# Optimization experiments

Measured on AMD Instinct MI355X. Metric: run time of the kernel, lower is better.

## Reference

```python
import jax, jax.numpy as jnp
import numpy as np

B, S, E, H = 2, 1024, 4096, 16
D = E // H          # head_dim = 256
RD = 64             # rotary_dim
# Quantization scales (alpha of the int8 GEMM epilogues)
A_QKV = 1.2e-4      # W8A8B8O8 q/k/v projection output scale
A_QK = 2e-4         # BMM_S8T_S8N_F32T alpha (= q_scale * k_scale)
A_PV = 1.0 / 127.0  # BMM_S8T_S8N_S8T alpha (probs quantized by *127)
A_O = 0.01          # W8A8BFP32OFP32 out_proj alpha


def setup_inputs() -> dict:
    key = jax.random.key(0)
    ks = jax.random.split(key, 9)
    ri = lambda k, shp: jax.random.randint(k, shp, -127, 128).astype(jnp.float32)
    return {
        "hidden_states": ri(ks[0], (B, S, E)),   # int8-valued activations
        "Wq": ri(ks[1], (E, E)),
        "Wk": ri(ks[2], (E, E)),
        "Wv": ri(ks[3], (E, E)),
        "Wo": ri(ks[4], (E, E)),
        "bq": ri(ks[5], (E,)),
        "bk": ri(ks[6], (E,)),
        "bv": ri(ks[7], (E,)),
        "bo": jax.random.normal(ks[8], (E,), dtype=jnp.float32) * 0.02,  # fp32 bias
    }


def _linear_i8(x, W, b, alpha):
    # W8A8B8O8Linear: int8 GEMM, scaled, +int8 bias, round+saturate to int8
    y = alpha * (x @ W.T) + b
    return jnp.clip(jnp.round(y), -128, 127)


def _rotate_every_two(x):
    x1 = x[..., ::2]
    x2 = x[..., 1::2]
    return jnp.stack((-x2, x1), axis=-1).reshape(x.shape)


def _apply_rotary(x, sin, cos):
    # duplicate_interleave == repeat each column twice; broadcast over [B, S, H, rd]
    sin = jnp.repeat(sin, 2, axis=-1)[None, :, None, :]
    cos = jnp.repeat(cos, 2, axis=-1)[None, :, None, :]
    r = x * cos + _rotate_every_two(x) * sin
    # torch: clamp(-128,127).to(int8) -> truncate toward zero
    return jnp.trunc(jnp.clip(r, -128.0, 127.0))


def reference(hidden_states, Wq, Wk, Wv, Wo, bq, bk, bv, bo):
    q = _linear_i8(hidden_states, Wq, bq, A_QKV).reshape(B, S, H, D)
    k = _linear_i8(hidden_states, Wk, bk, A_QKV).reshape(B, S, H, D)
    v = _linear_i8(hidden_states, Wv, bv, A_QKV).reshape(B, S, H, D)
    v = v.transpose(0, 2, 1, 3)  # [B, H, S, D]

    # fixed_pos_embedding over rotary_dim
    inv_freq = 1.0 / (10000.0 ** (jnp.arange(0, RD, 2, dtype=jnp.float32) / RD))
    t = jnp.arange(S, dtype=jnp.float32)
    sinusoid = t[:, None] * inv_freq[None, :]   # [S, RD/2]
    sin, cos = jnp.sin(sinusoid), jnp.cos(sinusoid)

    q = jnp.concatenate([_apply_rotary(q[..., :RD], sin, cos), q[..., RD:]], axis=-1)
    k = jnp.concatenate([_apply_rotary(k[..., :RD], sin, cos), k[..., RD:]], axis=-1)
    q = q.transpose(0, 2, 1, 3)  # [B, H, S, D]
    k = k.transpose(0, 2, 1, 3)

    w = A_QK * jnp.einsum('bhqd,bhkd->bhqk', q, k)
    causal = jnp.tril(jnp.ones((S, S), dtype=bool))[None, None]
    w = jnp.where(causal, w, jnp.finfo(jnp.float32).min)
    w = w / jnp.sqrt(jnp.float32(D))  # scale_attn = sqrt(head_dim)
    p = jnp.round(jax.nn.softmax(w, axis=-1) * 127.0)  # int8-valued probs

    # pv_bmm: int8 probs x int8 values -> scaled, round+saturate to int8
    o = jnp.clip(jnp.round(A_PV * jnp.einsum('bhqk,bhkd->bhqd', p, v)), -128, 127)
    o = o.transpose(0, 2, 1, 3).reshape(B, S, E)  # merge heads

    # out_proj: W8A8BFP32OFP32 -> fp32 output
    return A_O * (o @ Wo.T) + bo
```

## Files before the change

### kernel.cpp

```cpp
#include <hip/hip_runtime.h>
#include <hip/hip_bf16.h>

typedef int int32x4 __attribute__((ext_vector_type(4)));
typedef signed char i8;

#define B_ 2
#define S_ 1024
#define E_ 4096
#define H_ 16
#define D_ 256

#define MFMA_I8(a, b, c) __builtin_amdgcn_mfma_i32_16x16x64_i8((a), (b), (c), 0, 0, 0)

__device__ __forceinline__ int32x4 ld16(const void* p) {
    return *reinterpret_cast<const int32x4*>(p);
}

__device__ __forceinline__ void gload16(const void* g, void* l) {
    __builtin_amdgcn_global_load_lds(
        (const __attribute__((address_space(1))) void*)g,
        (__attribute__((address_space(3))) void*)l, 16, 0, 0);
}

#define WAIT_VM4()  asm volatile("s_waitcnt vmcnt(4)" ::: "memory")
#define WAIT_VM0()  asm volatile("s_waitcnt vmcnt(0)" ::: "memory")
#define WAIT_LGKM0() do { asm volatile("s_waitcnt lgkmcnt(0)" ::: "memory"); \
                          __builtin_amdgcn_sched_barrier(0); } while (0)

__device__ __forceinline__ int pack4(float4 f) {
    union { int w; i8 b[4]; } u;
    u.b[0] = (i8)f.x; u.b[1] = (i8)f.y; u.b[2] = (i8)f.z; u.b[3] = (i8)f.w;
    return u.w;
}

__global__ void k_f32_to_i8(const float* __restrict__ src, i8* __restrict__ dst, int n4) {
    int i = blockIdx.x * blockDim.x + threadIdx.x;
    if (i >= n4) return;
    reinterpret_cast<int*>(dst)[i] = pack4(reinterpret_cast<const float4*>(src)[i]);
}

__global__ void k_w_to_i8(const float* __restrict__ w0, const float* __restrict__ w1,
                          const float* __restrict__ w2, const float* __restrict__ w3,
                          i8* __restrict__ d0, i8* __restrict__ d1,
                          i8* __restrict__ d2, i8* __restrict__ d3, int n4) {
    int i = blockIdx.x * blockDim.x + threadIdx.x;
    if (i >= n4) return;
    const float* src = (blockIdx.y == 0) ? w0 : (blockIdx.y == 1) ? w1 : (blockIdx.y == 2) ? w2 : w3;
    i8* dst = (blockIdx.y == 0) ? d0 : (blockIdx.y == 1) ? d1 : (blockIdx.y == 2) ? d2 : d3;
    reinterpret_cast<int*>(dst)[i] = pack4(reinterpret_cast<const float4*>(src)[i]);
}

__global__ void k_sincos(float* __restrict__ sin_t, float* __restrict__ cos_t) {
    int idx = blockIdx.x * blockDim.x + threadIdx.x;
    if (idx >= S_ * 32) return;
    int s = idx >> 5, i = idx & 31;
    float ex = (float)(2 * i) / 64.0f;
    float invf = 1.0f / powf(10000.0f, ex);
    float arg = (float)s * invf;
    sin_t[idx] = (float)sin((double)arg);
    cos_t[idx] = (float)cos((double)arg);
}

template<bool OUT_I8>
__device__ __forceinline__ void gemm_core(
    const i8* __restrict__ X, const i8* __restrict__ W, const float* __restrict__ bias,
    void* __restrict__ out, float alpha, int M, int N, int K,
    i8 (&Alds)[3][8192], i8 (&Blds)[3][8192])
{
    const int nt = K >> 6;
    const int nwg = (M >> 7) * (N >> 7);
    const int q = nwg >> 3;
    const int lin = blockIdx.x;
    const int wg = (lin & 7) * q + (lin >> 3);
    const int nbm = M >> 7;
    const int m0 = (wg % nbm) * 128, n0 = (wg / nbm) * 128;

    const int tid = threadIdx.x, lane = tid & 63, wave = tid >> 6;
    const int wr = wave >> 1, wc = wave & 1, l4 = lane & 15, lh = lane >> 4;

    const int g4 = lh ^ ((l4 >> 1) & 3);
    const int aoff = (wr * 64 + l4) * 64 + g4 * 16;
    const int boff = (wc * 64 + l4) * 64 + g4 * 16;

    const int srow = tid >> 2;
    const int sg = (tid & 3) ^ ((tid >> 3) & 3);
    const i8* Asrc = X + (size_t)(m0 + srow) * K + sg * 16;
    const i8* Bsrc = W + (size_t)(n0 + srow) * K + sg * 16;
    const size_t rstep = (size_t)64 * K;
    const int ldst = wave * 1024;

#define STAGE_A(t_) do { int kb_ = (t_) * 64; i8* lb_ = Alds[(t_) % 3];      \
        gload16(Asrc + kb_,         lb_ + ldst);                             \
        gload16(Asrc + rstep + kb_, lb_ + 4096 + ldst); } while (0)
#define STAGE_B(t_) do { int kb_ = (t_) * 64; i8* lb_ = Blds[(t_) % 3];      \
        gload16(Bsrc + kb_,         lb_ + ldst);                             \
        gload16(Bsrc + rstep + kb_, lb_ + 4096 + ldst); } while (0)

    int32x4 acc[4][4];
#pragma unroll
    for (int m = 0; m < 4; ++m)
#pragma unroll
        for (int n = 0; n < 4; ++n) acc[m][n] = int32x4{0, 0, 0, 0};

    STAGE_A(0); STAGE_B(0);
    STAGE_A(1); STAGE_B(1);

    for (int t = 0; t < nt; ++t) {
        const i8* Ab = Alds[t % 3];
        const i8* Bb = Blds[t % 3];
        if (t + 1 < nt) { WAIT_VM4(); } else { WAIT_VM0(); }
        __builtin_amdgcn_s_barrier();

        int32x4 a0, a1, a2, a3, b0, b1, b2, b3;
        a0 = ld16(Ab + aoff);        a1 = ld16(Ab + aoff + 1024);
        a2 = ld16(Ab + aoff + 2048); a3 = ld16(Ab + aoff + 3072);
        b0 = ld16(Bb + boff);        b1 = ld16(Bb + boff + 1024);
        if (t + 2 < nt) STAGE_A(t + 2);
        __builtin_amdgcn_s_barrier();
        WAIT_LGKM0();
        __builtin_amdgcn_s_setprio(1);
        acc[0][0] = MFMA_I8(a0, b0, acc[0][0]);
        acc[1][0] = MFMA_I8(a1, b0, acc[1][0]);
        acc[2][0] = MFMA_I8(a2, b0, acc[2][0]);
        acc[3][0] = MFMA_I8(a3, b0, acc[3][0]);
        acc[0][1] = MFMA_I8(a0, b1, acc[0][1]);
        acc[1][1] = MFMA_I8(a1, b1, acc[1][1]);
        acc[2][1] = MFMA_I8(a2, b1, acc[2][1]);
        acc[3][1] = MFMA_I8(a3, b1, acc[3][1]);
        __builtin_amdgcn_s_setprio(0);
        __builtin_amdgcn_s_barrier();

        b2 = ld16(Bb + boff + 2048); b3 = ld16(Bb + boff + 3072);
        if (t + 2 < nt) STAGE_B(t + 2);
        __builtin_amdgcn_s_barrier();
        WAIT_LGKM0();
        __builtin_amdgcn_s_setprio(1);
        acc[0][2] = MFMA_I8(a0, b2, acc[0][2]);
        acc[1][2] = MFMA_I8(a1, b2, acc[1][2]);
        acc[2][2] = MFMA_I8(a2, b2, acc[2][2]);
        acc[3][2] = MFMA_I8(a3, b2, acc[3][2]);
        acc[0][3] = MFMA_I8(a0, b3, acc[0][3]);
        acc[1][3] = MFMA_I8(a1, b3, acc[1][3]);
        acc[2][3] = MFMA_I8(a2, b3, acc[2][3]);
        acc[3][3] = MFMA_I8(a3, b3, acc[3][3]);
        __builtin_amdgcn_s_setprio(0);
    }
#undef STAGE_A
#undef STAGE_B

#pragma unroll
    for (int m = 0; m < 4; ++m)
#pragma unroll
        for (int n = 0; n < 4; ++n)
#pragma unroll
            for (int r = 0; r < 4; ++r) {
                int grow = m0 + wr * 64 + m * 16 + lh * 4 + r;
                int gcol = n0 + wc * 64 + n * 16 + l4;
                float y = alpha * (float)acc[m][n][r] + bias[gcol];
                if (OUT_I8) {
                    float v = rintf(y);
                    v = fminf(fmaxf(v, -128.0f), 127.0f);
                    reinterpret_cast<i8*>(out)[(size_t)grow * N + gcol] = (i8)v;
                } else {
                    reinterpret_cast<float*>(out)[(size_t)grow * N + gcol] = y;
                }
            }
}

__global__ __launch_bounds__(256) void k_gemm_qkv(
    const i8* __restrict__ X,
    const i8* __restrict__ w0, const i8* __restrict__ w1, const i8* __restrict__ w2,
    const float* __restrict__ b0, const float* __restrict__ b1, const float* __restrict__ b2,
    i8* __restrict__ o0, i8* __restrict__ o1, i8* __restrict__ o2,
    float alpha, int M, int N, int K)
{
    __shared__ __align__(16) i8 Alds[3][8192];
    __shared__ __align__(16) i8 Blds[3][8192];
    int z = blockIdx.z;
    const i8* W = (z == 0) ? w0 : (z == 1) ? w1 : w2;
    const float* bias = (z == 0) ? b0 : (z == 1) ? b1 : b2;
    i8* out = (z == 0) ? o0 : (z == 1) ? o1 : o2;
    gemm_core<true>(X, W, bias, out, alpha, M, N, K, Alds, Blds);
}

__global__ __launch_bounds__(256) void k_gemm_out(
    const i8* __restrict__ X, const i8* __restrict__ W, const float* __restrict__ bias,
    float* __restrict__ out, float alpha, int M, int N, int K)
{
    __shared__ __align__(16) i8 Alds[3][8192];
    __shared__ __align__(16) i8 Blds[3][8192];
    gemm_core<false>(X, W, bias, out, alpha, M, N, K, Alds, Blds);
}

__global__ void k_rope(const i8* __restrict__ qin, const i8* __restrict__ kin,
                       i8* __restrict__ qout, i8* __restrict__ kout,
                       const float* __restrict__ sin_t, const float* __restrict__ cos_t)
{
    const i8* in = blockIdx.y ? kin : qin;
    i8* outp = blockIdx.y ? kout : qout;
    int row = blockIdx.x * 2 + (threadIdx.x >> 7);
    int i = threadIdx.x & 127;
    int b = row / (S_ * H_);
    int s = (row / H_) % S_;
    int h = row % H_;
    const i8* src = in + (size_t)row * D_ + i * 2;
    i8 x1 = src[0], x2 = src[1];
    i8 o1, o2;
    if (i < 32) {
        float c = cos_t[s * 32 + i], sn = sin_t[s * 32 + i];
        float f1 = (float)x1, f2 = (float)x2;
        float r0 = __fadd_rn(__fmul_rn(f1, c), __fmul_rn(-f2, sn));
        float r1 = __fadd_rn(__fmul_rn(f2, c), __fmul_rn(f1, sn));
        r0 = truncf(fminf(fmaxf(r0, -128.0f), 127.0f));
        r1 = truncf(fminf(fmaxf(r1, -128.0f), 127.0f));
        o1 = (i8)r0; o2 = (i8)r1;
    } else { o1 = x1; o2 = x2; }
    size_t ob = ((size_t)(b * H_ + h) * S_ + s) * D_ + i * 2;
    outp[ob] = o1; outp[ob + 1] = o2;
}

__global__ void k_vtrans(const i8* __restrict__ vin, i8* __restrict__ vout) {
    __shared__ int tile[64][17];
    int bh = blockIdx.z;
    int b = bh >> 4, h = bh & 15;
    int s0 = blockIdx.x * 64, d0 = blockIdx.y * 64;
    int t = threadIdx.x;
    {
        int sr = t >> 2, dq = (t & 3) * 16;
        int32x4 v = ld16(vin + ((size_t)(b * S_ + s0 + sr) * H_ + h) * D_ + d0 + dq);
#pragma unroll
        for (int j = 0; j < 4; ++j) tile[sr][dq / 4 + j] = v[j];
    }
    __syncthreads();
    {
        int dr = t >> 2, sq = (t & 3) * 16;
        union { int32x4 v; i8 b[16]; } u;
        const i8* tb = reinterpret_cast<const i8*>(tile);
#pragma unroll
        for (int j = 0; j < 16; ++j) u.b[j] = tb[(sq + j) * 68 + dr];
        *reinterpret_cast<int32x4*>(vout + ((size_t)bh * D_ + d0 + dr) * S_ + s0 + sq) = u.v;
    }
}

struct AttnShared {
    float slx[4][32];
    float r127[32];
    __align__(16) i8 plds[32][80];
};

__device__ __forceinline__ void attn_chunk(int qc, int bh, int tid,
    const i8* __restrict__ Qh, const i8* __restrict__ Kb, const i8* __restrict__ Vb,
    i8* __restrict__ O, AttnShared& sh)
{
    const float C2 = 1.25e-5f * 1.44269504088896f;
    const float APV = 1.0f / 127.0f;
    const int lane = tid & 63, wave = tid >> 6;
    const int l4 = lane & 15, lh = lane >> 4;
    const i8* Qb = Qh + (size_t)(qc * 32) * D_;
    const int nt = (qc * 32 + 31) / 64 + 1;

    int32x4 aq[2][4];
#pragma unroll
    for (int m = 0; m < 2; ++m)
#pragma unroll
        for (int kk = 0; kk < 4; ++kk)
            aq[m][kk] = ld16(Qb + (size_t)(m * 16 + l4) * D_ + kk * 64 + lh * 16);

    float sum_[2][4];
#pragma unroll
    for (int m = 0; m < 2; ++m)
#pragma unroll
        for (int r = 0; r < 4; ++r) sum_[m][r] = 0.0f;

    for (int kt = 0; kt < nt; ++kt) {
        int cb = kt * 64 + wave * 16;
        int32x4 acc0 = int32x4{0,0,0,0}, acc1 = int32x4{0,0,0,0};
#pragma unroll
        for (int kk = 0; kk < 4; ++kk) {
            int32x4 bf = ld16(Kb + (size_t)(cb + l4) * D_ + kk * 64 + lh * 16);
            acc0 = MFMA_I8(aq[0][kk], bf, acc0);
            acc1 = MFMA_I8(aq[1][kk], bf, acc1);
        }
        int gcol = cb + l4;
#pragma unroll
        for (int m = 0; m < 2; ++m) {
            int32x4 accm = m ? acc1 : acc0;
#pragma unroll
            for (int r = 0; r < 4; ++r) {
                int grow = qc * 32 + m * 16 + lh * 4 + r;
                float e = (gcol <= grow) ? exp2f((float)accm[r] * C2) : 0.0f;
                sum_[m][r] += e;
            }
        }
    }

#pragma unroll
    for (int m = 0; m < 2; ++m)
#pragma unroll
        for (int r = 0; r < 4; ++r) {
            float s = sum_[m][r];
            s += __shfl_xor(s, 1);
            s += __shfl_xor(s, 2);
            s += __shfl_xor(s, 4);
            s += __shfl_xor(s, 8);
            if (l4 == 0) sh.slx[wave][m * 16 + lh * 4 + r] = s;
        }
    __syncthreads();
    if (tid < 32)
        sh.r127[tid] = 127.0f /
            (sh.slx[0][tid] + sh.slx[1][tid] + sh.slx[2][tid] + sh.slx[3][tid]);
    __syncthreads();

    int32x4 oacc[2][4];
#pragma unroll
    for (int m = 0; m < 2; ++m)
#pragma unroll
        for (int n = 0; n < 4; ++n) oacc[m][n] = int32x4{0, 0, 0, 0};

    for (int kt = 0; kt < nt; ++kt) {
        int cb = kt * 64 + wave * 16;
        int32x4 acc0 = int32x4{0,0,0,0}, acc1 = int32x4{0,0,0,0};
#pragma unroll
        for (int kk = 0; kk < 4; ++kk) {
            int32x4 bf = ld16(Kb + (size_t)(cb + l4) * D_ + kk * 64 + lh * 16);
            acc0 = MFMA_I8(aq[0][kk], bf, acc0);
            acc1 = MFMA_I8(aq[1][kk], bf, acc1);
        }
        int gcol = cb + l4;
        i8 pv[2][4];
#pragma unroll
        for (int m = 0; m < 2; ++m) {
            int32x4 accm = m ? acc1 : acc0;
#pragma unroll
            for (int r = 0; r < 4; ++r) {
                int rowi = m * 16 + lh * 4 + r;
                int grow = qc * 32 + rowi;
                float e = (gcol <= grow) ? exp2f((float)accm[r] * C2) : 0.0f;
                pv[m][r] = (i8)(int)rintf(e * sh.r127[rowi]);
            }
        }
        __syncthreads();
#pragma unroll
        for (int m = 0; m < 2; ++m)
#pragma unroll
            for (int r = 0; r < 4; ++r)
                sh.plds[m * 16 + lh * 4 + r][wave * 16 + l4] = pv[m][r];
        __syncthreads();
        int32x4 a0 = ld16(&sh.plds[l4][lh * 16]);
        int32x4 a1 = ld16(&sh.plds[16 + l4][lh * 16]);
#pragma unroll
        for (int n = 0; n < 4; ++n) {
            int32x4 bf = ld16(Vb + (size_t)(wave * 64 + n * 16 + l4) * S_ + kt * 64 + lh * 16);
            oacc[0][n] = MFMA_I8(a0, bf, oacc[0][n]);
            oacc[1][n] = MFMA_I8(a1, bf, oacc[1][n]);
        }
    }

    int b = bh >> 4, h = bh & 15;
#pragma unroll
    for (int m = 0; m < 2; ++m)
#pragma unroll
        for (int r = 0; r < 4; ++r) {
            int s = qc * 32 + m * 16 + lh * 4 + r;
#pragma unroll
            for (int n = 0; n < 4; ++n) {
                float o = rintf(APV * (float)oacc[m][n][r]);
                o = fminf(fmaxf(o, -128.0f), 127.0f);
                O[((size_t)(b * S_ + s) * H_ + h) * D_ + wave * 64 + n * 16 + l4] = (i8)o;
            }
        }
}

__global__ __launch_bounds__(256) void k_attn(const i8* __restrict__ Q, const i8* __restrict__ K,
                                              const i8* __restrict__ V, i8* __restrict__ O)
{
    __shared__ AttnShared sh;
    int bh = blockIdx.x;
    int p = blockIdx.y;
    int tid = threadIdx.x;
    const i8* Qh = Q + (size_t)bh * S_ * D_;
    const i8* Kb = K + (size_t)bh * S_ * D_;
    const i8* Vb = V + (size_t)bh * D_ * S_;
    attn_chunk((S_ / 32 - 1) - p, bh, tid, Qh, Kb, Vb, O, sh);
    attn_chunk(p, bh, tid, Qh, Kb, Vb, O, sh);
}

extern "C" void kernel_launch(void* const* d_in, const int* in_sizes, int n_in,
                              void* d_out, int out_size, void* d_ws, size_t ws_size,
                              hipStream_t stream) {
    const float* hs = (const float*)d_in[0];
    const float* Wq = (const float*)d_in[1];
    const float* Wk = (const float*)d_in[2];
    const float* Wv = (const float*)d_in[3];
    const float* Wo = (const float*)d_in[4];
    const float* bq = (const float*)d_in[5];
    const float* bk = (const float*)d_in[6];
    const float* bv = (const float*)d_in[7];
    const float* bo = (const float*)d_in[8];
    float* out = (float*)d_out;

    size_t off = 0;
    char* wsb = (char*)d_ws;
    auto carve = [&](size_t bytes) { char* p = wsb + off; off += (bytes + 255) & ~(size_t)255; return p; };
    const size_t ME = (size_t)B_ * S_ * E_;
    const size_t EE = (size_t)E_ * E_;
    i8* x8  = (i8*)carve(ME);
    i8* wq8 = (i8*)carve(EE);
    i8* wk8 = (i8*)carve(EE);
    i8* wv8 = (i8*)carve(EE);
    i8* wo8 = (i8*)carve(EE);
    i8* q8  = (i8*)carve(ME);
    i8* k8  = (i8*)carve(ME);
    i8* v8  = (i8*)carve(ME);
    i8* qr  = (i8*)carve(ME);
    i8* kr  = (i8*)carve(ME);
    i8* vt  = (i8*)carve(ME);
    i8* o8  = (i8*)carve(ME);
    float* sin_t = (float*)carve((size_t)S_ * 32 * 4);
    float* cos_t = (float*)carve((size_t)S_ * 32 * 4);

    int n4_me = (int)(ME / 4), n4_ee = (int)(EE / 4);
    k_f32_to_i8<<<(n4_me + 255) / 256, 256, 0, stream>>>(hs, x8, n4_me);
    k_w_to_i8<<<dim3((n4_ee + 255) / 256, 4), 256, 0, stream>>>(
        Wq, Wk, Wv, Wo, wq8, wk8, wv8, wo8, n4_ee);
    k_sincos<<<(S_ * 32 + 255) / 256, 256, 0, stream>>>(sin_t, cos_t);

    const int M = B_ * S_, N = E_, Kd = E_;
    const int nwg = (M / 128) * (N / 128);
    k_gemm_qkv<<<dim3(nwg, 1, 3), 256, 0, stream>>>(
        x8, wq8, wk8, wv8, bq, bk, bv, q8, k8, v8, 0.00012f, M, N, Kd);

    k_rope<<<dim3((B_ * S_ * H_) / 2, 2), 256, 0, stream>>>(q8, k8, qr, kr, sin_t, cos_t);
    k_vtrans<<<dim3(S_ / 64, D_ / 64, B_ * H_), 256, 0, stream>>>(v8, vt);
    k_attn<<<dim3(B_ * H_, S_ / 64), 256, 0, stream>>>(qr, kr, vt, o8);

    k_gemm_out<<<nwg, 256, 0, stream>>>(o8, wo8, bo, out, 0.01f, M, N, Kd);
}
```

Baseline: 314.6 us.

## Enlarge GEMM tile to 256x128 with 512-thread blocks and unified LDS buffer

The int8 GEMMs for QKV and out-projection now use 256x128 output tiles computed by 8 waves (512 threads) instead of 128x128 with 4 waves. The A and B stages share one triple-buffered LDS region, so each B tile loaded from global memory is reused by twice as many rows. The staging loads per thread and the vmcnt wait thresholds are adjusted, and the MFMA order is rearranged so each half-phase covers two A fragments against all four B fragments. The aim is to cut global and L2 traffic per output element. In exchange the grid has half as many workgroups and each uses about 72KB of LDS, which may reduce occupancy and load balance across CUs.

```diff
diff --git a/kernel.cpp b/kernel.cpp
--- a/kernel.cpp
+++ b/kernel.cpp
@@ -22,7 +22,7 @@
         (__attribute__((address_space(3))) void*)l, 16, 0, 0);
 }
 
-#define WAIT_VM4()  asm volatile("s_waitcnt vmcnt(4)" ::: "memory")
+#define WAIT_VM3()  asm volatile("s_waitcnt vmcnt(3)" ::: "memory")
 #define WAIT_VM0()  asm volatile("s_waitcnt vmcnt(0)" ::: "memory")
 #define WAIT_LGKM0() do { asm volatile("s_waitcnt lgkmcnt(0)" ::: "memory"); \
                           __builtin_amdgcn_sched_barrier(0); } while (0)
@@ -64,37 +64,36 @@
 template<bool OUT_I8>
 __device__ __forceinline__ void gemm_core(
     const i8* __restrict__ X, const i8* __restrict__ W, const float* __restrict__ bias,
-    void* __restrict__ out, float alpha, int M, int N, int K,
-    i8 (&Alds)[3][8192], i8 (&Blds)[3][8192])
+    void* __restrict__ out, float alpha, int M, int N, int K, i8* lds)
 {
     const int nt = K >> 6;
-    const int nwg = (M >> 7) * (N >> 7);
+    const int nwg = (M >> 8) * (N >> 7);
     const int q = nwg >> 3;
     const int lin = blockIdx.x;
     const int wg = (lin & 7) * q + (lin >> 3);
-    const int nbm = M >> 7;
-    const int m0 = (wg % nbm) * 128, n0 = (wg / nbm) * 128;
+    const int nbm = M >> 8;
+    const int m0 = (wg % nbm) * 256, n0 = (wg / nbm) * 128;
 
     const int tid = threadIdx.x, lane = tid & 63, wave = tid >> 6;
     const int wr = wave >> 1, wc = wave & 1, l4 = lane & 15, lh = lane >> 4;
 
     const int g4 = lh ^ ((l4 >> 1) & 3);
     const int aoff = (wr * 64 + l4) * 64 + g4 * 16;
-    const int boff = (wc * 64 + l4) * 64 + g4 * 16;
+    const int boff = 16384 + (wc * 64 + l4) * 64 + g4 * 16;
 
     const int srow = tid >> 2;
     const int sg = (tid & 3) ^ ((tid >> 3) & 3);
     const i8* Asrc = X + (size_t)(m0 + srow) * K + sg * 16;
     const i8* Bsrc = W + (size_t)(n0 + srow) * K + sg * 16;
-    const size_t rstep = (size_t)64 * K;
+    const size_t rstep = (size_t)128 * K;
     const int ldst = wave * 1024;
 
-#define STAGE_A(t_) do { int kb_ = (t_) * 64; i8* lb_ = Alds[(t_) % 3];      \
+#define BUF(t_) (lds + ((t_) % 3) * 24576)
+#define STAGE_A(t_) do { int kb_ = (t_) * 64; i8* lb_ = BUF(t_);             \
         gload16(Asrc + kb_,         lb_ + ldst);                             \
-        gload16(Asrc + rstep + kb_, lb_ + 4096 + ldst); } while (0)
-#define STAGE_B(t_) do { int kb_ = (t_) * 64; i8* lb_ = Blds[(t_) % 3];      \
-        gload16(Bsrc + kb_,         lb_ + ldst);                             \
-        gload16(Bsrc + rstep + kb_, lb_ + 4096 + ldst); } while (0)
+        gload16(Asrc + rstep + kb_, lb_ + 8192 + ldst); } while (0)
+#define STAGE_B(t_) do { int kb_ = (t_) * 64; i8* lb_ = BUF(t_);             \
+        gload16(Bsrc + kb_,         lb_ + 16384 + ldst); } while (0)
 
     int32x4 acc[4][4];
 #pragma unroll
@@ -106,45 +105,45 @@
     STAGE_A(1); STAGE_B(1);
 
     for (int t = 0; t < nt; ++t) {
-        const i8* Ab = Alds[t % 3];
-        const i8* Bb = Blds[t % 3];
-        if (t + 1 < nt) { WAIT_VM4(); } else { WAIT_VM0(); }
+        const i8* Tb = BUF(t);
+        if (t + 1 < nt) { WAIT_VM3(); } else { WAIT_VM0(); }
         __builtin_amdgcn_s_barrier();
 
         int32x4 a0, a1, a2, a3, b0, b1, b2, b3;
-        a0 = ld16(Ab + aoff);        a1 = ld16(Ab + aoff + 1024);
-        a2 = ld16(Ab + aoff + 2048); a3 = ld16(Ab + aoff + 3072);
-        b0 = ld16(Bb + boff);        b1 = ld16(Bb + boff + 1024);
+        a0 = ld16(Tb + aoff);        a1 = ld16(Tb + aoff + 1024);
+        b0 = ld16(Tb + boff);        b1 = ld16(Tb + boff + 1024);
+        b2 = ld16(Tb + boff + 2048); b3 = ld16(Tb + boff + 3072);
         if (t + 2 < nt) STAGE_A(t + 2);
         __builtin_amdgcn_s_barrier();
         WAIT_LGKM0();
         __builtin_amdgcn_s_setprio(1);
         acc[0][0] = MFMA_I8(a0, b0, acc[0][0]);
+        acc[0][1] = MFMA_I8(a0, b1, acc[0][1]);
+        acc[0][2] = MFMA_I8(a0, b2, acc[0][2]);
+        acc[0][3] = MFMA_I8(a0, b3, acc[0][3]);
         acc[1][0] = MFMA_I8(a1, b0, acc[1][0]);
-        acc[2][0] = MFMA_I8(a2, b0, acc[2][0]);
-        acc[3][0] = MFMA_I8(a3, b0, acc[3][0]);
-        acc[0][1] = MFMA_I8(a0, b1, acc[0][1]);
         acc[1][1] = MFMA_I8(a1, b1, acc[1][1]);
-        acc[2][1] = MFMA_I8(a2, b1, acc[2][1]);
-        acc[3][1] = MFMA_I8(a3, b1, acc[3][1]);
+        acc[1][2] = MFMA_I8(a1, b2, acc[1][2]);
+        acc[1][3] = MFMA_I8(a1, b3, acc[1][3]);
         __builtin_amdgcn_s_setprio(0);
         __builtin_amdgcn_s_barrier();
 
-        b2 = ld16(Bb + boff + 2048); b3 = ld16(Bb + boff + 3072);
+        a2 = ld16(Tb + aoff + 2048); a3 = ld16(Tb + aoff + 3072);
         if (t + 2 < nt) STAGE_B(t + 2);
         __builtin_amdgcn_s_barrier();
         WAIT_LGKM0();
         __builtin_amdgcn_s_setprio(1);
-        acc[0][2] = MFMA_I8(a0, b2, acc[0][2]);
-        acc[1][2] = MFMA_I8(a1, b2, acc[1][2]);
+        acc[2][0] = MFMA_I8(a2, b0, acc[2][0]);
+        acc[2][1] = MFMA_I8(a2, b1, acc[2][1]);
         acc[2][2] = MFMA_I8(a2, b2, acc[2][2]);
+        acc[2][3] = MFMA_I8(a2, b3, acc[2][3]);
+        acc[3][0] = MFMA_I8(a3, b0, acc[3][0]);
+        acc[3][1] = MFMA_I8(a3, b1, acc[3][1]);
         acc[3][2] = MFMA_I8(a3, b2, acc[3][2]);
-        acc[0][3] = MFMA_I8(a0, b3, acc[0][3]);
-        acc[1][3] = MFMA_I8(a1, b3, acc[1][3]);
-        acc[2][3] = MFMA_I8(a2, b3, acc[2][3]);
         acc[3][3] = MFMA_I8(a3, b3, acc[3][3]);
         __builtin_amdgcn_s_setprio(0);
     }
+#undef BUF
 #undef STAGE_A
 #undef STAGE_B
 
@@ -167,29 +166,27 @@
             }
 }
 
-__global__ __launch_bounds__(256) void k_gemm_qkv(
+__global__ __launch_bounds__(512, 4) void k_gemm_qkv(
     const i8* __restrict__ X,
     const i8* __restrict__ w0, const i8* __restrict__ w1, const i8* __restrict__ w2,
     const float* __restrict__ b0, const float* __restrict__ b1, const float* __restrict__ b2,
     i8* __restrict__ o0, i8* __restrict__ o1, i8* __restrict__ o2,
     float alpha, int M, int N, int K)
 {
-    __shared__ __align__(16) i8 Alds[3][8192];
-    __shared__ __align__(16) i8 Blds[3][8192];
+    __shared__ __align__(16) i8 lds[3 * 24576];
     int z = blockIdx.z;
     const i8* W = (z == 0) ? w0 : (z == 1) ? w1 : w2;
     const float* bias = (z == 0) ? b0 : (z == 1) ? b1 : b2;
     i8* out = (z == 0) ? o0 : (z == 1) ? o1 : o2;
-    gemm_core<true>(X, W, bias, out, alpha, M, N, K, Alds, Blds);
-}
-
-__global__ __launch_bounds__(256) void k_gemm_out(
+    gemm_core<true>(X, W, bias, out, alpha, M, N, K, lds);
+}
+
+__global__ __launch_bounds__(512, 4) void k_gemm_out(
     const i8* __restrict__ X, const i8* __restrict__ W, const float* __restrict__ bias,
     float* __restrict__ out, float alpha, int M, int N, int K)
 {
-    __shared__ __align__(16) i8 Alds[3][8192];
-    __shared__ __align__(16) i8 Blds[3][8192];
-    gemm_core<false>(X, W, bias, out, alpha, M, N, K, Alds, Blds);
+    __shared__ __align__(16) i8 lds[3 * 24576];
+    gemm_core<false>(X, W, bias, out, alpha, M, N, K, lds);
 }
 
 __global__ void k_rope(const i8* __restrict__ qin, const i8* __restrict__ kin,
@@ -426,13 +423,13 @@
     k_sincos<<<(S_ * 32 + 255) / 256, 256, 0, stream>>>(sin_t, cos_t);
 
     const int M = B_ * S_, N = E_, Kd = E_;
-    const int nwg = (M / 128) * (N / 128);
-    k_gemm_qkv<<<dim3(nwg, 1, 3), 256, 0, stream>>>(
+    const int nwg = (M / 256) * (N / 128);
+    k_gemm_qkv<<<dim3(nwg, 1, 3), 512, 0, stream>>>(
         x8, wq8, wk8, wv8, bq, bk, bv, q8, k8, v8, 0.00012f, M, N, Kd);
 
     k_rope<<<dim3((B_ * S_ * H_) / 2, 2), 256, 0, stream>>>(q8, k8, qr, kr, sin_t, cos_t);
     k_vtrans<<<dim3(S_ / 64, D_ / 64, B_ * H_), 256, 0, stream>>>(v8, vt);
     k_attn<<<dim3(B_ * H_, S_ / 64), 256, 0, stream>>>(qr, kr, vt, o8);
 
-    k_gemm_out<<<nwg, 256, 0, stream>>>(o8, wo8, bo, out, 0.01f, M, N, Kd);
-}
+    k_gemm_out<<<nwg, 512, 0, stream>>>(o8, wo8, bo, out, 0.01f, M, N, Kd);
+}
```

Result: faster. 301.1 us (-4.3%).
